# Performance work log

Hardware: AMD Instinct MI355X
Metric: run time of the kernel (lower is better)

The kernel has to match this reference:

```python
import jax, jax.numpy as jnp
import numpy as np

B, T, I, H, O = 512, 1024, 80, 160, 1


def setup_inputs() -> dict:
    key = jax.random.key(0)
    ks = jax.random.split(key, 11)
    s = 1.0 / np.sqrt(H)  # pytorch default init scale
    return {
        "x": jax.random.normal(ks[0], (B, T, I), dtype=jnp.float32),
        "W_ih0": jax.random.normal(ks[1], (4 * H, I), dtype=jnp.float32) * s,
        "W_hh0": jax.random.normal(ks[2], (4 * H, H), dtype=jnp.float32) * s,
        "b_ih0": jax.random.normal(ks[3], (4 * H,), dtype=jnp.float32) * s,
        "b_hh0": jax.random.normal(ks[4], (4 * H,), dtype=jnp.float32) * s,
        "W_ih1": jax.random.normal(ks[5], (4 * H, H), dtype=jnp.float32) * s,
        "W_hh1": jax.random.normal(ks[6], (4 * H, H), dtype=jnp.float32) * s,
        "b_ih1": jax.random.normal(ks[7], (4 * H,), dtype=jnp.float32) * s,
        "b_hh1": jax.random.normal(ks[8], (4 * H,), dtype=jnp.float32) * s,
        "W_out": jax.random.normal(ks[9], (O, H), dtype=jnp.float32) * s,
        "b_out": jax.random.normal(ks[10], (O,), dtype=jnp.float32) * s,
    }


def _lstm_cell(xt, h, c, W_ih, W_hh, b_ih, b_hh):
    # gates: [B, 4H], pytorch order i, f, g, o
    gates = xt @ W_ih.T + b_ih + h @ W_hh.T + b_hh
    i, f, g, o = jnp.split(gates, 4, axis=-1)
    c_new = jax.nn.sigmoid(f) * c + jax.nn.sigmoid(i) * jnp.tanh(g)
    h_new = jax.nn.sigmoid(o) * jnp.tanh(c_new)
    return h_new, c_new


def reference(x, W_ih0, W_hh0, b_ih0, b_hh0, W_ih1, W_hh1, b_ih1, b_hh1, W_out, b_out):
    Bx = x.shape[0]
    h0 = jnp.zeros((Bx, H), x.dtype)
    init = (h0, h0, h0, h0)  # (h_l0, c_l0, h_l1, c_l1)

    def step(carry, xt):
        h0_, c0_, h1_, c1_ = carry
        h0n, c0n = _lstm_cell(xt, h0_, c0_, W_ih0, W_hh0, b_ih0, b_hh0)
        h1n, c1n = _lstm_cell(h0n, h1_, c1_, W_ih1, W_hh1, b_ih1, b_hh1)
        y = jax.nn.relu(h1n @ W_out.T + b_out)  # [B, O]
        return (h0n, c0n, h1n, c1n), y

    xs = jnp.swapaxes(x, 0, 1)  # [T, B, I]
    _, ys = jax.lax.scan(step, init, xs)  # [T, B, O]
    return jnp.swapaxes(ys, 0, 1)  # [B, T, O]
```

## Files before the change

### kernel.cpp

```cpp
#include <hip/hip_runtime.h>
#include <stdint.h>


#define TT 1024
#define BATCH 512
#define II 80
#define HH 160

constexpr int BB    = 16;
constexpr int NGRP  = BATCH / BB;
constexpr int NW    = 8;
constexpr int NTHR  = NW * 64;
constexpr int NTILE = 5;
constexpr int DEPTH = 32;
constexpr int HP    = 168;

typedef __attribute__((ext_vector_type(8))) short s8b;
typedef __attribute__((ext_vector_type(4))) float f4;

constexpr int SLOT_U64 = 960;
constexpr size_t OFF_RING = 4096;
constexpr size_t RING_STRIDE = (size_t)DEPTH * SLOT_U64 * 8;

constexpr int HSH_OFF = 81920;
constexpr int H0L_OFF = 92672;
constexpr int YP_OFF  = 103424;
constexpr int BS_OFF  = 104448;
constexpr int WO_OFF  = 107008;
constexpr int SMEM_SZ = 107648;

__device__ __forceinline__ short f2bf(float x){
  uint32_t u = __builtin_bit_cast(uint32_t, x);
  u = (u + 0x7FFFu + ((u >> 16) & 1u)) >> 16;
  return (short)u;
}
__device__ __forceinline__ float sigf(float x){ return 1.f/(1.f+__expf(-x)); }
__device__ __forceinline__ float tanh_(float x){ return 1.f - 2.f/(__expf(2.f*x)+1.f); }

__device__ __forceinline__ f4 mfma16(s8b a, s8b b, f4 c){
  return __builtin_amdgcn_mfma_f32_16x16x32_bf16(a, b, c, 0, 0, 0);
}

template<int CTRL>
__device__ __forceinline__ float qperm(float v){
  return __builtin_bit_cast(float,
    __builtin_amdgcn_mov_dpp(__builtin_bit_cast(int, v), CTRL, 0xf, 0xf, true));
}
__device__ __forceinline__ void qtrans(f4 acc, int q, float gv[4]){
  float a0=acc[0], a1=acc[1], a2=acc[2], a3=acc[3];
  float s0 = q==0?a0 : q==1?a1 : q==2?a2 : a3;
  float s1 = q==0?a3 : q==1?a0 : q==2?a1 : a2;
  float s2 = q==0?a2 : q==1?a3 : q==2?a0 : a1;
  float s3 = q==0?a1 : q==1?a2 : q==2?a3 : a0;
  float r0 = s0;
  float r1 = qperm<0x39>(s1);
  float r2 = qperm<0x4E>(s2);
  float r3 = qperm<0x93>(s3);
  gv[0] = q==0?r0 : q==1?r3 : q==2?r2 : r1;
  gv[1] = q==0?r1 : q==1?r0 : q==2?r3 : r2;
  gv[2] = q==0?r2 : q==1?r1 : q==2?r0 : r3;
  gv[3] = q==0?r3 : q==1?r2 : q==2?r1 : r0;
}

__device__ __forceinline__ s8b pack8(float4 a, float4 b){
  s8b r;
  r[0]=f2bf(a.x); r[1]=f2bf(a.y); r[2]=f2bf(a.z); r[3]=f2bf(a.w);
  r[4]=f2bf(b.x); r[5]=f2bf(b.y); r[6]=f2bf(b.z); r[7]=f2bf(b.w);
  return r;
}
__device__ __forceinline__ float4 ld4(const float* p){ return *(const float4*)p; }
__device__ __forceinline__ s8b wfrag(const float* p){ return pack8(ld4(p), ld4(p+4)); }

__device__ __forceinline__ void st64(unsigned long long* p, unsigned long long v){
  __hip_atomic_store(p, v, __ATOMIC_RELAXED, __HIP_MEMORY_SCOPE_AGENT);
}
__device__ __forceinline__ unsigned long long ld64(const unsigned long long* p){
  return __hip_atomic_load(p, __ATOMIC_RELAXED, __HIP_MEMORY_SCOPE_AGENT);
}
__device__ __forceinline__ void poll_ge(int* p, int& shadow, int target, int lane){
  while (shadow < target){
    int v = 0;
    if (lane == 0) v = __hip_atomic_load(p, __ATOMIC_ACQUIRE, __HIP_MEMORY_SCOPE_AGENT);
    shadow = __shfl(v, 0, 64);
    if (shadow < target) __builtin_amdgcn_s_sleep(2);
  }
}

__global__ __launch_bounds__(NTHR, 1)
void lstm2(const float* __restrict__ x,
           const float* __restrict__ Wih0, const float* __restrict__ Whh0,
           const float* __restrict__ bih0, const float* __restrict__ bhh0,
           const float* __restrict__ Wih1, const float* __restrict__ Whh1,
           const float* __restrict__ bih1, const float* __restrict__ bhh1,
           const float* __restrict__ Wout, const float* __restrict__ bout,
           float* __restrict__ out, char* __restrict__ ws)
{
  extern __shared__ char smem[];
  const int tid = threadIdx.x;
  const int w   = tid >> 6;
  const int l   = tid & 63;
  const int lq  = l >> 4;
  const int lr  = l & 15;
  const int q   = l & 3;
  const int h2  = (l >> 2) & 3;
  const int stage = blockIdx.x >> 5;
  const int gid   = blockIdx.x & 31;
  const int b0    = gid * BB;

  int* prog = (int*)ws + gid;
  unsigned long long* ring =
      (unsigned long long*)(ws + OFF_RING + (size_t)gid * RING_STRIDE);

  short* hsh = (short*)(smem + HSH_OFF);
  const s8b zf = {};

  if (stage == 0){
    s8b Wh[NTILE][5], Wi2[NTILE];
    float bias0[NTILE];
    #pragma unroll
    for (int s = 0; s < NTILE; ++s){
      const int ct = w + 8*s;
      const int wrow = q*HH + 4*ct + h2;
      bias0[s] = bih0[wrow] + bhh0[wrow];
      #pragma unroll
      for (int kt = 0; kt < 2; ++kt)
        *(s8b*)(smem + ((w*10 + s*2 + kt) << 10) + (l << 4)) =
            wfrag(Wih0 + (size_t)wrow*II + kt*32 + lq*8);
      Wi2[s] = (lq < 2) ? wfrag(Wih0 + (size_t)wrow*II + 64 + lq*8) : zf;
      #pragma unroll
      for (int kt = 0; kt < 5; ++kt)
        Wh[s][kt] = wfrag(Whh0 + (size_t)wrow*HH + kt*32 + lq*8);
    }
    __syncthreads();

    s8b xa[3], h0a[5];
    #pragma unroll
    for (int kt = 0; kt < 5; ++kt) h0a[kt] = zf;
    float c0[NTILE] = {0.f,0.f,0.f,0.f,0.f};

    const float* xb = x + (size_t)(b0 + lr) * TT * II;
    {
      float4 a0 = ld4(xb + lq*8),      a1 = ld4(xb + lq*8 + 4);
      float4 a2 = ld4(xb + 32 + lq*8), a3 = ld4(xb + 32 + lq*8 + 4);
      const float* x2 = (lq < 2) ? xb + 64 + lq*8 : xb;
      float4 a4 = ld4(x2), a5 = ld4(x2 + 4);
      xa[0] = pack8(a0,a1); xa[1] = pack8(a2,a3);
      xa[2] = (lq < 2) ? pack8(a4,a5) : zf;
    }
    f4 accx[NTILE];
    #pragma unroll
    for (int s = 0; s < NTILE; ++s){
      accx[s] = (f4){bias0[s], bias0[s], bias0[s], bias0[s]};
      accx[s] = mfma16(xa[0], *(const s8b*)(smem + ((w*10 + s*2 + 0) << 10) + (l << 4)), accx[s]);
      accx[s] = mfma16(xa[1], *(const s8b*)(smem + ((w*10 + s*2 + 1) << 10) + (l << 4)), accx[s]);
      accx[s] = mfma16(xa[2], Wi2[s], accx[s]);
    }

    int credB = 0;
    for (int t = 0; t < TT; ++t){
      const int tn = (t+1 < TT) ? t+1 : t;
      const float* xr = xb + (size_t)tn * II;
      float4 n0 = ld4(xr + lq*8),      n1 = ld4(xr + lq*8 + 4);
      float4 n2 = ld4(xr + 32 + lq*8), n3 = ld4(xr + 32 + lq*8 + 4);
      const float* x2 = (lq < 2) ? xr + 64 + lq*8 : xr;
      float4 n4 = ld4(x2), n5 = ld4(x2 + 4);

      if (t >= DEPTH && credB < t - DEPTH + 1)
        poll_ge(prog, credB, t - DEPTH + 1, l);

      short* hb = hsh + (t&1)*16*HP;
      #pragma unroll
      for (int kt = 0; kt < 5; ++kt)
        #pragma unroll
        for (int s = 0; s < NTILE; ++s)
          accx[s] = mfma16(h0a[kt], Wh[s][kt], accx[s]);
      #pragma unroll
      for (int s = 0; s < NTILE; ++s){
        float gv[4]; qtrans(accx[s], q, gv);
        const float cn = sigf(gv[1])*c0[s] + sigf(gv[0])*tanh_(gv[2]);
        c0[s] = cn;
        const float h = sigf(gv[3])*tanh_(cn);
        hb[(lq*4 + q)*HP + 4*(w + 8*s) + h2] = f2bf(h);
      }
      __syncthreads();
      #pragma unroll
      for (int kt = 0; kt < 5; ++kt)
        h0a[kt] = *(const s8b*)&hb[lr*HP + kt*32 + lq*8];
      if (w < 5){
        const s8b hf = h0a[w];
        const unsigned long long tg = (unsigned long long)t;
        unsigned long long u0 = (unsigned long long)(unsigned short)hf[0]
                              | ((unsigned long long)(unsigned short)hf[1] << 16)
                              | ((unsigned long long)(unsigned short)hf[2] << 32)
                              | (tg << 48);
        unsigned long long u1 = (unsigned long long)(unsigned short)hf[3]
                              | ((unsigned long long)(unsigned short)hf[4] << 16)
                              | ((unsigned long long)(unsigned short)hf[5] << 32)
                              | (tg << 48);
        unsigned long long u2 = (unsigned long long)(unsigned short)hf[6]
                              | ((unsigned long long)(unsigned short)hf[7] << 16)
                              | (tg << 32) | (tg << 48);
        unsigned long long* dst = ring + (size_t)(t & (DEPTH-1))*SLOT_U64 + (w*64 + l)*3;
        st64(dst, u0); st64(dst+1, u1); st64(dst+2, u2);
      }
      xa[0] = pack8(n0,n1); xa[1] = pack8(n2,n3);
      xa[2] = (lq < 2) ? pack8(n4,n5) : zf;
      #pragma unroll
      for (int s = 0; s < NTILE; ++s){
        accx[s] = (f4){bias0[s], bias0[s], bias0[s], bias0[s]};
        accx[s] = mfma16(xa[0], *(const s8b*)(smem + ((w*10 + s*2 + 0) << 10) + (l << 4)), accx[s]);
        accx[s] = mfma16(xa[1], *(const s8b*)(smem + ((w*10 + s*2 + 1) << 10) + (l << 4)), accx[s]);
        accx[s] = mfma16(xa[2], Wi2[s], accx[s]);
      }
    }
  }
  else {
    short* h0l = (short*)(smem + H0L_OFF);
    float* ypart = (float*)(smem + YP_OFF);
    float* biassh = (float*)(smem + BS_OFF);
    float* woutsh = (float*)(smem + WO_OFF);
    for (int i = tid; i < 640; i += NTHR){
      const int ct = i >> 4, r = i & 15;
      const int row = (r&3)*HH + 4*ct + (r>>2);
      biassh[i] = bih1[row] + bhh1[row];
    }
    for (int i = tid; i < HH; i += NTHR) woutsh[i] = Wout[i];
    s8b Wi[NTILE][3], Wh[NTILE][5];
    float woutv[NTILE];
    #pragma unroll
    for (int s = 0; s < NTILE; ++s){
      const int ct = w + 8*s;
      const int wrow = q*HH + 4*ct + h2;
      woutv[s] = Wout[4*ct + h2];
      #pragma unroll
      for (int kt = 0; kt < 5; ++kt)
        Wh[s][kt] = wfrag(Whh1 + (size_t)wrow*HH + kt*32 + lq*8);
      #pragma unroll
      for (int kt = 0; kt < 3; ++kt)
        Wi[s][kt] = wfrag(Wih1 + (size_t)wrow*HH + kt*32 + lq*8);
      #pragma unroll
      for (int kt = 3; kt < 5; ++kt)
        *(s8b*)(smem + ((w*10 + s*2 + (kt-3)) << 10) + (l << 4)) =
            wfrag(Wih1 + (size_t)wrow*HH + kt*32 + lq*8);
    }
    const float bo = bout[0];
    s8b h1a[5];
    #pragma unroll
    for (int kt = 0; kt < 5; ++kt) h1a[kt] = zf;
    float c1[NTILE] = {0.f,0.f,0.f,0.f,0.f};

    unsigned long long in0 = 0, in1 = 0, in2 = 0;
    if (w < 5){
      const unsigned long long* src = ring + (w*64 + l)*3;
      in0 = ld64(src); in1 = ld64(src+1); in2 = ld64(src+2);
      bool ok = ((int)(in0>>48)==0) && ((int)(in1>>48)==0) && ((int)(in2>>48)==0);
      while (__ballot(ok) != ~0ull){
        __builtin_amdgcn_s_sleep(1);
        in0 = ld64(src); in1 = ld64(src+1); in2 = ld64(src+2);
        ok = ((int)(in0>>48)==0) && ((int)(in1>>48)==0) && ((int)(in2>>48)==0);
      }
      s8b v;
      v[0]=(short)in0; v[1]=(short)(in0>>16); v[2]=(short)(in0>>32);
      v[3]=(short)in1; v[4]=(short)(in1>>16); v[5]=(short)(in1>>32);
      v[6]=(short)in2; v[7]=(short)(in2>>16);
      *(s8b*)&h0l[lr*HP + w*32 + lq*8] = v;
      const unsigned long long* p1 = ring + (size_t)(1 & (DEPTH-1))*SLOT_U64 + (w*64 + l)*3;
      in0 = ld64(p1); in1 = ld64(p1+1); in2 = ld64(p1+2);
    }
    __syncthreads();

    f4 accx[NTILE];
    {
      const short* hp = h0l;
      #pragma unroll
      for (int s = 0; s < NTILE; ++s){
        const float b = biassh[(w + 8*s)*16 + lr];
        accx[s] = (f4){b, b, b, b};
      }
      #pragma unroll
      for (int kt = 0; kt < 3; ++kt){
        const s8b hf = *(const s8b*)&hp[lr*HP + kt*32 + lq*8];
        #pragma unroll
        for (int s = 0; s < NTILE; ++s) accx[s] = mfma16(hf, Wi[s][kt], accx[s]);
      }
      #pragma unroll
      for (int kt = 3; kt < 5; ++kt){
        const s8b hf = *(const s8b*)&hp[lr*HP + kt*32 + lq*8];
        #pragma unroll
        for (int s = 0; s < NTILE; ++s)
          accx[s] = mfma16(hf, *(const s8b*)(smem + ((w*10 + s*2 + (kt-3)) << 10) + (l << 4)), accx[s]);
      }
    }

    for (int t = 0; t < TT; ++t){
      short* hb = hsh + (t&1)*16*HP;
      #pragma unroll
      for (int kt = 0; kt < 5; ++kt)
        #pragma unroll
        for (int s = 0; s < NTILE; ++s)
          accx[s] = mfma16(h1a[kt], Wh[s][kt], accx[s]);

      if (w < 5 && t+1 < TT){
        const int tg = t+1;
        const unsigned long long* src =
            ring + (size_t)(tg & (DEPTH-1))*SLOT_U64 + (w*64 + l)*3;
        bool ok = ((int)(in0>>48)==tg) && ((int)(in1>>48)==tg) && ((int)(in2>>48)==tg);
        while (__ballot(ok) != ~0ull){
          __builtin_amdgcn_s_sleep(1);
          in0 = ld64(src); in1 = ld64(src+1); in2 = ld64(src+2);
          ok = ((int)(in0>>48)==tg) && ((int)(in1>>48)==tg) && ((int)(in2>>48)==tg);
        }
        s8b v;
        v[0]=(short)in0; v[1]=(short)(in0>>16); v[2]=(short)(in0>>32);
        v[3]=(short)in1; v[4]=(short)(in1>>16); v[5]=(short)(in1>>32);
        v[6]=(short)in2; v[7]=(short)(in2>>16);
        *(s8b*)&h0l[((t+1)&1)*16*HP + lr*HP + w*32 + lq*8] = v;
      }

      float ysum = 0.f;
      #pragma unroll
      for (int s = 0; s < NTILE; ++s){
        float gv[4]; qtrans(accx[s], q, gv);
        const float cn = sigf(gv[1])*c1[s] + sigf(gv[0])*tanh_(gv[2]);
        c1[s] = cn;
        const float h = sigf(gv[3])*tanh_(cn);
        hb[(lq*4 + q)*HP + 4*(w + 8*s) + h2] = f2bf(h);
        ysum += h * woutv[s];
      }
      ysum += __shfl_xor(ysum, 4, 64);
      ysum += __shfl_xor(ysum, 8, 64);
      if ((l & 12) == 0) ypart[(t&1)*128 + w*16 + lq*4 + q] = ysum;

      __syncthreads();
      #pragma unroll
      for (int kt = 0; kt < 5; ++kt)
        h1a[kt] = *(const s8b*)&hb[lr*HP + kt*32 + lq*8];
      if (w == 0 && l < 16){
        float s_ = bo;
        #pragma unroll
        for (int ww = 0; ww < NW; ++ww) s_ += ypart[(t&1)*128 + ww*16 + l];
        out[(size_t)(b0 + l)*TT + t] = fmaxf(s_, 0.f);
      }
      {
        const short* hp = h0l + ((t+1)&1)*16*HP;
        #pragma unroll
        for (int s = 0; s < NTILE; ++s){
          const float b = biassh[(w + 8*s)*16 + lr];
          accx[s] = (f4){b, b, b, b};
        }
        #pragma unroll
        for (int kt = 0; kt < 3; ++kt){
          const s8b hf = *(const s8b*)&hp[lr*HP + kt*32 + lq*8];
          #pragma unroll
          for (int s = 0; s < NTILE; ++s) accx[s] = mfma16(hf, Wi[s][kt], accx[s]);
        }
        #pragma unroll
        for (int kt = 3; kt < 5; ++kt){
          const s8b hf = *(const s8b*)&hp[lr*HP + kt*32 + lq*8];
          #pragma unroll
          for (int s = 0; s < NTILE; ++s)
            accx[s] = mfma16(hf, *(const s8b*)(smem + ((w*10 + s*2 + (kt-3)) << 10) + (l << 4)), accx[s]);
        }
      }
      if (w < 5 && t+2 < TT){
        const unsigned long long* p =
            ring + (size_t)((t+2) & (DEPTH-1))*SLOT_U64 + (w*64 + l)*3;
        in0 = ld64(p); in1 = ld64(p+1); in2 = ld64(p+2);
      }
      if (((t & 7) == 7) && tid == 0)
        __hip_atomic_store(prog, t+1, __ATOMIC_RELEASE, __HIP_MEMORY_SCOPE_AGENT);
    }
  }
}

extern "C" void kernel_launch(void* const* d_in, const int* in_sizes, int n_in,
                              void* d_out, int out_size, void* d_ws, size_t ws_size,
                              hipStream_t stream)
{
  (void)in_sizes; (void)n_in; (void)out_size; (void)ws_size;
  (void)hipFuncSetAttribute(reinterpret_cast<const void*>(lstm2),
                            hipFuncAttributeMaxDynamicSharedMemorySize, SMEM_SZ);
  (void)hipMemsetAsync(d_ws, 0, 4096, stream);
  lstm2<<<dim3(NGRP*2), dim3(NTHR), SMEM_SZ, stream>>>(
      (const float*)d_in[0],
      (const float*)d_in[1], (const float*)d_in[2],
      (const float*)d_in[3], (const float*)d_in[4],
      (const float*)d_in[5], (const float*)d_in[6],
      (const float*)d_in[7], (const float*)d_in[8],
      (const float*)d_in[9], (const float*)d_in[10],
      (float*)d_out, (char*)d_ws);
}
```

Before: 5.349 ms.

## Swap MFMA operands to drop gate transpose, stage x via LDS, coalesce ring

Swaps the A/B operands of the gate MFMAs so each lane's accumulator already holds the four gates for its own hidden unit. This removes the DPP-based quad transpose and changes the h store, bias and output-reduction layouts to match. The x input is now loaded by a single wave, converted to bf16 and staged in double-buffered LDS, instead of every wave loading and packing it. Ring slots are changed to a structure-of-arrays layout for coalesced 64-bit stores and loads, and the division is replaced by a raw v_rcp_f32. Risks include lower reciprocal precision and extra load latency on wave 7.

```diff
diff --git a/kernel.cpp b/kernel.cpp
--- a/kernel.cpp
+++ b/kernel.cpp
@@ -14,8 +14,10 @@
 constexpr int NTILE = 5;
 constexpr int DEPTH = 32;
 constexpr int HP    = 168;
+constexpr int XP    = 88;
 
 typedef __attribute__((ext_vector_type(8))) short s8b;
+typedef __attribute__((ext_vector_type(4))) short s4b;
 typedef __attribute__((ext_vector_type(4))) float f4;
 
 constexpr int SLOT_U64 = 960;
@@ -26,7 +28,6 @@
 constexpr int H0L_OFF = 92672;
 constexpr int YP_OFF  = 103424;
 constexpr int BS_OFF  = 104448;
-constexpr int WO_OFF  = 107008;
 constexpr int SMEM_SZ = 107648;
 
 __device__ __forceinline__ short f2bf(float x){
@@ -34,32 +35,16 @@
   u = (u + 0x7FFFu + ((u >> 16) & 1u)) >> 16;
   return (short)u;
 }
-__device__ __forceinline__ float sigf(float x){ return 1.f/(1.f+__expf(-x)); }
-__device__ __forceinline__ float tanh_(float x){ return 1.f - 2.f/(__expf(2.f*x)+1.f); }
+__device__ __forceinline__ float rcpf(float x){
+  float r;
+  asm("v_rcp_f32 %0, %1" : "=v"(r) : "v"(x));
+  return r;
+}
+__device__ __forceinline__ float sigf(float x){ return rcpf(1.f + __expf(-x)); }
+__device__ __forceinline__ float tanh_(float x){ return 1.f - 2.f*rcpf(__expf(2.f*x)+1.f); }
 
 __device__ __forceinline__ f4 mfma16(s8b a, s8b b, f4 c){
   return __builtin_amdgcn_mfma_f32_16x16x32_bf16(a, b, c, 0, 0, 0);
-}
-
-template<int CTRL>
-__device__ __forceinline__ float qperm(float v){
-  return __builtin_bit_cast(float,
-    __builtin_amdgcn_mov_dpp(__builtin_bit_cast(int, v), CTRL, 0xf, 0xf, true));
-}
-__device__ __forceinline__ void qtrans(f4 acc, int q, float gv[4]){
-  float a0=acc[0], a1=acc[1], a2=acc[2], a3=acc[3];
-  float s0 = q==0?a0 : q==1?a1 : q==2?a2 : a3;
-  float s1 = q==0?a3 : q==1?a0 : q==2?a1 : a2;
-  float s2 = q==0?a2 : q==1?a3 : q==2?a0 : a1;
-  float s3 = q==0?a1 : q==1?a2 : q==2?a3 : a0;
-  float r0 = s0;
-  float r1 = qperm<0x39>(s1);
-  float r2 = qperm<0x4E>(s2);
-  float r3 = qperm<0x93>(s3);
-  gv[0] = q==0?r0 : q==1?r3 : q==2?r2 : r1;
-  gv[1] = q==0?r1 : q==1?r0 : q==2?r3 : r2;
-  gv[2] = q==0?r2 : q==1?r1 : q==2?r0 : r3;
-  gv[3] = q==0?r3 : q==1?r2 : q==2?r1 : r0;
 }
 
 __device__ __forceinline__ s8b pack8(float4 a, float4 b){
@@ -106,6 +91,7 @@
   const int stage = blockIdx.x >> 5;
   const int gid   = blockIdx.x & 31;
   const int b0    = gid * BB;
+  const int li    = w*64 + l;
 
   int* prog = (int*)ws + gid;
   unsigned long long* ring =
@@ -115,13 +101,17 @@
   const s8b zf = {};
 
   if (stage == 0){
+    short* xsh = (short*)(smem + H0L_OFF);
     s8b Wh[NTILE][5], Wi2[NTILE];
-    float bias0[NTILE];
+    f4 biasv[NTILE];
     #pragma unroll
     for (int s = 0; s < NTILE; ++s){
       const int ct = w + 8*s;
       const int wrow = q*HH + 4*ct + h2;
-      bias0[s] = bih0[wrow] + bhh0[wrow];
+      const int u = 4*ct + lq;
+      #pragma unroll
+      for (int g = 0; g < 4; ++g)
+        biasv[s][g] = bih0[g*HH + u] + bhh0[g*HH + u];
       #pragma unroll
       for (int kt = 0; kt < 2; ++kt)
         *(s8b*)(smem + ((w*10 + s*2 + kt) << 10) + (l << 4)) =
@@ -131,39 +121,46 @@
       for (int kt = 0; kt < 5; ++kt)
         Wh[s][kt] = wfrag(Whh0 + (size_t)wrow*HH + kt*32 + lq*8);
     }
+    if (w == 7){
+      const float* xp = x + (size_t)(b0 + lr) * TT * II + (l>>4)*20;
+      short* xd = xsh + lr*XP + (l>>4)*20;
+      #pragma unroll
+      for (int i = 0; i < 5; ++i){
+        float4 a = ld4(xp + i*4);
+        s4b p; p[0]=f2bf(a.x); p[1]=f2bf(a.y); p[2]=f2bf(a.z); p[3]=f2bf(a.w);
+        *(s4b*)(xd + i*4) = p;
+      }
+    }
     __syncthreads();
 
-    s8b xa[3], h0a[5];
+    s8b h0a[5];
     #pragma unroll
     for (int kt = 0; kt < 5; ++kt) h0a[kt] = zf;
     float c0[NTILE] = {0.f,0.f,0.f,0.f,0.f};
 
-    const float* xb = x + (size_t)(b0 + lr) * TT * II;
+    s8b xa[3];
     {
-      float4 a0 = ld4(xb + lq*8),      a1 = ld4(xb + lq*8 + 4);
-      float4 a2 = ld4(xb + 32 + lq*8), a3 = ld4(xb + 32 + lq*8 + 4);
-      const float* x2 = (lq < 2) ? xb + 64 + lq*8 : xb;
-      float4 a4 = ld4(x2), a5 = ld4(x2 + 4);
-      xa[0] = pack8(a0,a1); xa[1] = pack8(a2,a3);
-      xa[2] = (lq < 2) ? pack8(a4,a5) : zf;
+      const short* xr = xsh + lr*XP;
+      xa[0] = *(const s8b*)&xr[lq*8];
+      xa[1] = *(const s8b*)&xr[32 + lq*8];
+      xa[2] = (lq < 2) ? *(const s8b*)&xr[64 + lq*8] : zf;
     }
     f4 accx[NTILE];
     #pragma unroll
     for (int s = 0; s < NTILE; ++s){
-      accx[s] = (f4){bias0[s], bias0[s], bias0[s], bias0[s]};
-      accx[s] = mfma16(xa[0], *(const s8b*)(smem + ((w*10 + s*2 + 0) << 10) + (l << 4)), accx[s]);
-      accx[s] = mfma16(xa[1], *(const s8b*)(smem + ((w*10 + s*2 + 1) << 10) + (l << 4)), accx[s]);
-      accx[s] = mfma16(xa[2], Wi2[s], accx[s]);
+      accx[s] = biasv[s];
+      accx[s] = mfma16(*(const s8b*)(smem + ((w*10 + s*2 + 0) << 10) + (l << 4)), xa[0], accx[s]);
+      accx[s] = mfma16(*(const s8b*)(smem + ((w*10 + s*2 + 1) << 10) + (l << 4)), xa[1], accx[s]);
+      accx[s] = mfma16(Wi2[s], xa[2], accx[s]);
     }
 
     int credB = 0;
     for (int t = 0; t < TT; ++t){
-      const int tn = (t+1 < TT) ? t+1 : t;
-      const float* xr = xb + (size_t)tn * II;
-      float4 n0 = ld4(xr + lq*8),      n1 = ld4(xr + lq*8 + 4);
-      float4 n2 = ld4(xr + 32 + lq*8), n3 = ld4(xr + 32 + lq*8 + 4);
-      const float* x2 = (lq < 2) ? xr + 64 + lq*8 : xr;
-      float4 n4 = ld4(x2), n5 = ld4(x2 + 4);
+      float4 xl0, xl1, xl2, xl3, xl4;
+      if (w == 7 && t+1 < TT){
+        const float* xp = x + (size_t)(b0 + lr) * TT * II + (size_t)(t+1)*II + (l>>4)*20;
+        xl0 = ld4(xp); xl1 = ld4(xp+4); xl2 = ld4(xp+8); xl3 = ld4(xp+12); xl4 = ld4(xp+16);
+      }
 
       if (t >= DEPTH && credB < t - DEPTH + 1)
         poll_ge(prog, credB, t - DEPTH + 1, l);
@@ -173,14 +170,22 @@
       for (int kt = 0; kt < 5; ++kt)
         #pragma unroll
         for (int s = 0; s < NTILE; ++s)
-          accx[s] = mfma16(h0a[kt], Wh[s][kt], accx[s]);
+          accx[s] = mfma16(Wh[s][kt], h0a[kt], accx[s]);
       #pragma unroll
       for (int s = 0; s < NTILE; ++s){
-        float gv[4]; qtrans(accx[s], q, gv);
-        const float cn = sigf(gv[1])*c0[s] + sigf(gv[0])*tanh_(gv[2]);
+        const float cn = sigf(accx[s][1])*c0[s] + sigf(accx[s][0])*tanh_(accx[s][2]);
         c0[s] = cn;
-        const float h = sigf(gv[3])*tanh_(cn);
-        hb[(lq*4 + q)*HP + 4*(w + 8*s) + h2] = f2bf(h);
+        const float h = sigf(accx[s][3])*tanh_(cn);
+        hb[lr*HP + 4*(w + 8*s) + lq] = f2bf(h);
+      }
+      if (w == 7 && t+1 < TT){
+        short* xd = xsh + ((t+1)&1)*16*XP + lr*XP + (l>>4)*20;
+        float4 a[5] = {xl0, xl1, xl2, xl3, xl4};
+        #pragma unroll
+        for (int i = 0; i < 5; ++i){
+          s4b p; p[0]=f2bf(a[i].x); p[1]=f2bf(a[i].y); p[2]=f2bf(a[i].z); p[3]=f2bf(a[i].w);
+          *(s4b*)(xd + i*4) = p;
+        }
       }
       __syncthreads();
       #pragma unroll
@@ -200,38 +205,41 @@
         unsigned long long u2 = (unsigned long long)(unsigned short)hf[6]
                               | ((unsigned long long)(unsigned short)hf[7] << 16)
                               | (tg << 32) | (tg << 48);
-        unsigned long long* dst = ring + (size_t)(t & (DEPTH-1))*SLOT_U64 + (w*64 + l)*3;
-        st64(dst, u0); st64(dst+1, u1); st64(dst+2, u2);
-      }
-      xa[0] = pack8(n0,n1); xa[1] = pack8(n2,n3);
-      xa[2] = (lq < 2) ? pack8(n4,n5) : zf;
+        unsigned long long* sl = ring + (size_t)(t & (DEPTH-1))*SLOT_U64;
+        st64(sl + li, u0); st64(sl + 320 + li, u1); st64(sl + 640 + li, u2);
+      }
+      {
+        const short* xr = xsh + ((t+1)&1)*16*XP + lr*XP;
+        xa[0] = *(const s8b*)&xr[lq*8];
+        xa[1] = *(const s8b*)&xr[32 + lq*8];
+        xa[2] = (lq < 2) ? *(const s8b*)&xr[64 + lq*8] : zf;
+      }
       #pragma unroll
       for (int s = 0; s < NTILE; ++s){
-        accx[s] = (f4){bias0[s], bias0[s], bias0[s], bias0[s]};
-        accx[s] = mfma16(xa[0], *(const s8b*)(smem + ((w*10 + s*2 + 0) << 10) + (l << 4)), accx[s]);
-        accx[s] = mfma16(xa[1], *(const s8b*)(smem + ((w*10 + s*2 + 1) << 10) + (l << 4)), accx[s]);
-        accx[s] = mfma16(xa[2], Wi2[s], accx[s]);
+        accx[s] = biasv[s];
+        accx[s] = mfma16(*(const s8b*)(smem + ((w*10 + s*2 + 0) << 10) + (l << 4)), xa[0], accx[s]);
+        accx[s] = mfma16(*(const s8b*)(smem + ((w*10 + s*2 + 1) << 10) + (l << 4)), xa[1], accx[s]);
+        accx[s] = mfma16(Wi2[s], xa[2], accx[s]);
       }
     }
   }
   else {
     short* h0l = (short*)(smem + H0L_OFF);
     float* ypart = (float*)(smem + YP_OFF);
-    float* biassh = (float*)(smem + BS_OFF);
-    float* woutsh = (float*)(smem + WO_OFF);
-    for (int i = tid; i < 640; i += NTHR){
-      const int ct = i >> 4, r = i & 15;
-      const int row = (r&3)*HH + 4*ct + (r>>2);
-      biassh[i] = bih1[row] + bhh1[row];
-    }
-    for (int i = tid; i < HH; i += NTHR) woutsh[i] = Wout[i];
+    f4* bias4 = (f4*)(smem + BS_OFF);
+    for (int i = tid; i < HH; i += NTHR){
+      f4 b;
+      #pragma unroll
+      for (int g = 0; g < 4; ++g) b[g] = bih1[g*HH + i] + bhh1[g*HH + i];
+      bias4[i] = b;
+    }
     s8b Wi[NTILE][3], Wh[NTILE][5];
     float woutv[NTILE];
     #pragma unroll
     for (int s = 0; s < NTILE; ++s){
       const int ct = w + 8*s;
       const int wrow = q*HH + 4*ct + h2;
-      woutv[s] = Wout[4*ct + h2];
+      woutv[s] = Wout[4*ct + lq];
       #pragma unroll
       for (int kt = 0; kt < 5; ++kt)
         Wh[s][kt] = wfrag(Whh1 + (size_t)wrow*HH + kt*32 + lq*8);
@@ -251,12 +259,12 @@
 
     unsigned long long in0 = 0, in1 = 0, in2 = 0;
     if (w < 5){
-      const unsigned long long* src = ring + (w*64 + l)*3;
-      in0 = ld64(src); in1 = ld64(src+1); in2 = ld64(src+2);
+      const unsigned long long* src = ring;
+      in0 = ld64(src + li); in1 = ld64(src + 320 + li); in2 = ld64(src + 640 + li);
       bool ok = ((int)(in0>>48)==0) && ((int)(in1>>48)==0) && ((int)(in2>>48)==0);
       while (__ballot(ok) != ~0ull){
         __builtin_amdgcn_s_sleep(1);
-        in0 = ld64(src); in1 = ld64(src+1); in2 = ld64(src+2);
+        in0 = ld64(src + li); in1 = ld64(src + 320 + li); in2 = ld64(src + 640 + li);
         ok = ((int)(in0>>48)==0) && ((int)(in1>>48)==0) && ((int)(in2>>48)==0);
       }
       s8b v;
@@ -264,8 +272,8 @@
       v[3]=(short)in1; v[4]=(short)(in1>>16); v[5]=(short)(in1>>32);
       v[6]=(short)in2; v[7]=(short)(in2>>16);
       *(s8b*)&h0l[lr*HP + w*32 + lq*8] = v;
-      const unsigned long long* p1 = ring + (size_t)(1 & (DEPTH-1))*SLOT_U64 + (w*64 + l)*3;
-      in0 = ld64(p1); in1 = ld64(p1+1); in2 = ld64(p1+2);
+      const unsigned long long* p1 = ring + (size_t)(1 & (DEPTH-1))*SLOT_U64;
+      in0 = ld64(p1 + li); in1 = ld64(p1 + 320 + li); in2 = ld64(p1 + 640 + li);
     }
     __syncthreads();
 
@@ -273,22 +281,20 @@
     {
       const short* hp = h0l;
       #pragma unroll
-      for (int s = 0; s < NTILE; ++s){
-        const float b = biassh[(w + 8*s)*16 + lr];
-        accx[s] = (f4){b, b, b, b};
-      }
+      for (int s = 0; s < NTILE; ++s)
+        accx[s] = bias4[4*(w + 8*s) + lq];
       #pragma unroll
       for (int kt = 0; kt < 3; ++kt){
         const s8b hf = *(const s8b*)&hp[lr*HP + kt*32 + lq*8];
         #pragma unroll
-        for (int s = 0; s < NTILE; ++s) accx[s] = mfma16(hf, Wi[s][kt], accx[s]);
+        for (int s = 0; s < NTILE; ++s) accx[s] = mfma16(Wi[s][kt], hf, accx[s]);
       }
       #pragma unroll
       for (int kt = 3; kt < 5; ++kt){
         const s8b hf = *(const s8b*)&hp[lr*HP + kt*32 + lq*8];
         #pragma unroll
         for (int s = 0; s < NTILE; ++s)
-          accx[s] = mfma16(hf, *(const s8b*)(smem + ((w*10 + s*2 + (kt-3)) << 10) + (l << 4)), accx[s]);
+          accx[s] = mfma16(*(const s8b*)(smem + ((w*10 + s*2 + (kt-3)) << 10) + (l << 4)), hf, accx[s]);
       }
     }
 
@@ -298,16 +304,15 @@
       for (int kt = 0; kt < 5; ++kt)
         #pragma unroll
         for (int s = 0; s < NTILE; ++s)
-          accx[s] = mfma16(h1a[kt], Wh[s][kt], accx[s]);
+          accx[s] = mfma16(Wh[s][kt], h1a[kt], accx[s]);
 
       if (w < 5 && t+1 < TT){
         const int tg = t+1;
-        const unsigned long long* src =
-            ring + (size_t)(tg & (DEPTH-1))*SLOT_U64 + (w*64 + l)*3;
+        const unsigned long long* src = ring + (size_t)(tg & (DEPTH-1))*SLOT_U64;
         bool ok = ((int)(in0>>48)==tg) && ((int)(in1>>48)==tg) && ((int)(in2>>48)==tg);
         while (__ballot(ok) != ~0ull){
           __builtin_amdgcn_s_sleep(1);
-          in0 = ld64(src); in1 = ld64(src+1); in2 = ld64(src+2);
+          in0 = ld64(src + li); in1 = ld64(src + 320 + li); in2 = ld64(src + 640 + li);
           ok = ((int)(in0>>48)==tg) && ((int)(in1>>48)==tg) && ((int)(in2>>48)==tg);
         }
         s8b v;
@@ -320,16 +325,15 @@
       float ysum = 0.f;
       #pragma unroll
       for (int s = 0; s < NTILE; ++s){
-        float gv[4]; qtrans(accx[s], q, gv);
-        const float cn = sigf(gv[1])*c1[s] + sigf(gv[0])*tanh_(gv[2]);
+        const float cn = sigf(accx[s][1])*c1[s] + sigf(accx[s][0])*tanh_(accx[s][2]);
         c1[s] = cn;
-        const float h = sigf(gv[3])*tanh_(cn);
-        hb[(lq*4 + q)*HP + 4*(w + 8*s) + h2] = f2bf(h);
+        const float h = sigf(accx[s][3])*tanh_(cn);
+        hb[lr*HP + 4*(w + 8*s) + lq] = f2bf(h);
         ysum += h * woutv[s];
       }
-      ysum += __shfl_xor(ysum, 4, 64);
-      ysum += __shfl_xor(ysum, 8, 64);
-      if ((l & 12) == 0) ypart[(t&1)*128 + w*16 + lq*4 + q] = ysum;
+      ysum += __shfl_xor(ysum, 16, 64);
+      ysum += __shfl_xor(ysum, 32, 64);
+      if (l < 16) ypart[(t&1)*128 + w*16 + l] = ysum;
 
       __syncthreads();
       #pragma unroll
@@ -344,28 +348,26 @@
       {
         const short* hp = h0l + ((t+1)&1)*16*HP;
         #pragma unroll
-        for (int s = 0; s < NTILE; ++s){
-          const float b = biassh[(w + 8*s)*16 + lr];
-          accx[s] = (f4){b, b, b, b};
-        }
+        for (int s = 0; s < NTILE; ++s)
+          accx[s] = bias4[4*(w + 8*s) + lq];
         #pragma unroll
         for (int kt = 0; kt < 3; ++kt){
           const s8b hf = *(const s8b*)&hp[lr*HP + kt*32 + lq*8];
           #pragma unroll
-          for (int s = 0; s < NTILE; ++s) accx[s] = mfma16(hf, Wi[s][kt], accx[s]);
+          for (int s = 0; s < NTILE; ++s) accx[s] = mfma16(Wi[s][kt], hf, accx[s]);
         }
         #pragma unroll
         for (int kt = 3; kt < 5; ++kt){
           const s8b hf = *(const s8b*)&hp[lr*HP + kt*32 + lq*8];
           #pragma unroll
           for (int s = 0; s < NTILE; ++s)
-            accx[s] = mfma16(hf, *(const s8b*)(smem + ((w*10 + s*2 + (kt-3)) << 10) + (l << 4)), accx[s]);
+            accx[s] = mfma16(*(const s8b*)(smem + ((w*10 + s*2 + (kt-3)) << 10) + (l << 4)), hf, accx[s]);
         }
       }
       if (w < 5 && t+2 < TT){
         const unsigned long long* p =
-            ring + (size_t)((t+2) & (DEPTH-1))*SLOT_U64 + (w*64 + l)*3;
-        in0 = ld64(p); in1 = ld64(p+1); in2 = ld64(p+2);
+            ring + (size_t)((t+2) & (DEPTH-1))*SLOT_U64;
+        in0 = ld64(p + li); in1 = ld64(p + 320 + li); in2 = ld64(p + 640 + li);
       }
       if (((t & 7) == 7) && tid == 0)
         __hip_atomic_store(prog, t+1, __ATOMIC_RELEASE, __HIP_MEMORY_SCOPE_AGENT);
```

New measurement: 4.459 ms. -16.6%, faster.
